# Optimization experiments

Measured on AMD Instinct MI355X. Metric: run time of the kernel, lower is better.

The kernel has to match this reference:

```python
import jax, jax.numpy as jnp
import numpy as np

B, L, LH, D, H = 32, 512, 2048, 1024, 4
DK = D // H  # dot-attn head dim
NEG = -1e9


def _ln(x, g, b, eps=1e-5):
    m = x.mean(-1, keepdims=True)
    v = ((x - m) ** 2).mean(-1, keepdims=True)
    return (x - m) / jnp.sqrt(v + eps) * g + b


def setup_inputs() -> dict:
    key = jax.random.key(0)
    ks = jax.random.split(key, 16)
    s = 0.05
    inp = {
        "seq_emb": jax.random.normal(ks[0], (B, L, D), jnp.float32),
        "seq_mask": jnp.ones((B, L), jnp.float32),
        "his_seq_emb": jax.random.normal(ks[1], (B, LH, D), jnp.float32),
        "his_seq_mask": jnp.ones((B, LH), jnp.float32),
        # dot-product MHA (bias=True)
        "sa_wq": jax.random.normal(ks[2], (D, D), jnp.float32) * s,
        "sa_bq": jnp.zeros((D,), jnp.float32),
        "sa_wk": jax.random.normal(ks[3], (D, D), jnp.float32) * s,
        "sa_bk": jnp.zeros((D,), jnp.float32),
        "sa_wv": jax.random.normal(ks[4], (D, D), jnp.float32) * s,
        "sa_bv": jnp.zeros((D,), jnp.float32),
        "sa_wo": jax.random.normal(ks[5], (D, D), jnp.float32) * s,
        "sa_bo": jnp.zeros((D,), jnp.float32),
        # short LayerNorm
        "sn_g": jnp.ones((D,), jnp.float32),
        "sn_b": jnp.zeros((D,), jnp.float32),
        # additive MHA (h=1, bias=False)
        "aa_wq": jax.random.normal(ks[6], (D, D), jnp.float32) * s,
        "aa_wk": jax.random.normal(ks[7], (D, D), jnp.float32) * s,
        "aa_wv": jax.random.normal(ks[8], (D, D), jnp.float32) * s,
        "aa_wo": jax.random.normal(ks[9], (D, D), jnp.float32) * s,
        "aa_wa": jax.random.normal(ks[10], (D,), jnp.float32) * s,
        # long LayerNorm
        "ln_g": jnp.ones((D,), jnp.float32),
        "ln_b": jnp.zeros((D,), jnp.float32),
    }
    return inp


def reference(seq_emb, seq_mask, his_seq_emb, his_seq_mask,
              sa_wq, sa_bq, sa_wk, sa_bk, sa_wv, sa_bv, sa_wo, sa_bo,
              sn_g, sn_b, aa_wq, aa_wk, aa_wv, aa_wo, aa_wa, ln_g, ln_b):
    # ---- dot-product self attention over seq_emb (dropout = eval/no-op) ----
    def split_heads(x):  # (B,L,D) -> (B,H,L,DK)
        return x.reshape(B, -1, H, DK).transpose(0, 2, 1, 3)

    q = split_heads(seq_emb @ sa_wq + sa_bq)
    k = split_heads(seq_emb @ sa_wk + sa_bk)
    v = split_heads(seq_emb @ sa_wv + sa_bv)
    scores = jnp.einsum('bhqd,bhkd->bhqk', q, k) / jnp.sqrt(jnp.float32(DK))
    scores = jnp.where(seq_mask[:, None, None, :] == 0, NEG, scores)
    p_attn = jax.nn.softmax(scores, axis=-1)  # (B,H,L,L)
    ctx = jnp.einsum('bhqk,bhkd->bhqd', p_attn, v)
    ctx = ctx.transpose(0, 2, 1, 3).reshape(B, L, D)
    sa_out = ctx @ sa_wo + sa_bo

    poi_attn = _ln(sa_out, sn_g, sn_b) * seq_mask[:, :, None]
    poi_hidden = poi_attn.mean(axis=1, keepdims=True)  # (B,1,D)

    # ---- additive (Bahdanau) attention, h=1, Lq=1 ----
    aq = poi_hidden @ aa_wq        # (B,1,D)
    ak = his_seq_emb @ aa_wk       # (B,LH,D)
    av = his_seq_emb @ aa_wv       # (B,LH,D)
    feats = jnp.tanh(aq[:, :, None, :] + ak[:, None, :, :])  # (B,1,LH,D)
    a_scores = jnp.einsum('bqkd,d->bqk', feats, aa_wa)        # (B,1,LH)
    a_scores = jnp.where(his_seq_mask[:, None, :] == 0, NEG, a_scores)
    a_w = jax.nn.softmax(a_scores, axis=-1)
    a_ctx = jnp.einsum('bqk,bkd->bqd', a_w, av)               # (B,1,D)
    aa_out = a_ctx @ aa_wo

    his_poi_hidden = poi_hidden + _ln(aa_out, ln_g, ln_b)     # (B,1,D)

    attn_weight = p_attn[:, 0, :, :]                          # (B,L,L)
    seq_hidden = jnp.concatenate([poi_hidden, his_poi_hidden], axis=-1)[:, 0, :]  # (B,2D)
    return seq_hidden, attn_weight
```

## Files before the change

kernel.cpp:

```cpp
#include <hip/hip_runtime.h>

#define NEGV (-1000000000.0f)

typedef __attribute__((ext_vector_type(8))) short sh8;
typedef __attribute__((ext_vector_type(4))) short sh4;
typedef __attribute__((ext_vector_type(8))) __bf16 bf16x8;
typedef __attribute__((ext_vector_type(4))) float f32x4;

__device__ __forceinline__ float b2f(unsigned short u) {
  unsigned v = ((unsigned)u) << 16;
  return __builtin_bit_cast(float, v);
}
__device__ __forceinline__ unsigned short f2b(float f) {
  unsigned x = __builtin_bit_cast(unsigned, f);
  unsigned r = (x + 0x7fffu + ((x >> 16) & 1u)) >> 16;
  return (unsigned short)r;
}
__device__ __forceinline__ void g2l16(const void* g, void* l) {
  __builtin_amdgcn_global_load_lds((const __attribute__((address_space(1))) unsigned int*)g,
                                   (__attribute__((address_space(3))) unsigned int*)l, 16, 0, 0);
}
__device__ __forceinline__ f32x4 mfma16(bf16x8 a, bf16x8 b, f32x4 c) {
  return __builtin_amdgcn_mfma_f32_16x16x32_bf16(a, b, c, 0, 0, 0);
}
__device__ __forceinline__ float fast_tanh(float x) {
  x = fminf(fmaxf(x, -15.f), 15.f);
  float e = __expf(2.f * x);
  return (e - 1.f) / (e + 1.f);
}

__global__ void cvt_bf16(const float* __restrict__ src, unsigned short* __restrict__ dst, int n4) {
  int i = blockIdx.x * blockDim.x + threadIdx.x;
  int stride = gridDim.x * blockDim.x;
  for (; i < n4; i += stride) {
    float4 v = ((const float4*)src)[i];
    sh4 o;
    o[0] = (short)f2b(v.x); o[1] = (short)f2b(v.y);
    o[2] = (short)f2b(v.z); o[3] = (short)f2b(v.w);
    ((sh4*)dst)[i] = o;
  }
}

__global__ void tcvt(const float* __restrict__ src, unsigned short* __restrict__ dst) {
  __shared__ float tile[64][65];
  int bx = blockIdx.x, by = blockIdx.y;
  int tx = threadIdx.x & 63, ty = threadIdx.x >> 6;
#pragma unroll
  for (int i = 0; i < 16; ++i) {
    int r = i * 4 + ty;
    tile[r][tx] = src[(size_t)(by * 64 + r) * 1024 + bx * 64 + tx];
  }
  __syncthreads();
#pragma unroll
  for (int i = 0; i < 16; ++i) {
    int r = i * 4 + ty;
    dst[(size_t)(bx * 64 + r) * 1024 + by * 64 + tx] = f2b(tile[tx][r]);
  }
}

template<int EPI>
__global__ __launch_bounds__(512, 1)
void gemm256(const unsigned short* __restrict__ A, const unsigned short* __restrict__ Bt,
             int nbx,
             const float* __restrict__ b0, const float* __restrict__ b1,
             const float* __restrict__ b2,
             unsigned short* __restrict__ O0, unsigned short* __restrict__ O1,
             unsigned short* __restrict__ O2,
             const float* __restrict__ aq, const float* __restrict__ wa,
             float* __restrict__ sc)
{
  __shared__ char lds[131072];
  const int tid = threadIdx.x;
  const int w = tid >> 6, l = tid & 63;
  const int wm = w >> 2, wn = w & 3;
  const int lr = l & 15, g = l >> 4;
  const int kg16 = g * 16;

  const int wg = blockIdx.x;
  const int cpx = gridDim.x >> 3;
  const int wgid = (wg & 7) * cpx + (wg >> 3);
  const int bx = wgid % nbx, by = wgid / nbx;
  const size_t m0 = (size_t)by * 256;
  const int n0 = bx * 256;

  f32x4 acc[8][4] = {};

  const int srow = tid >> 2, sk = (tid & 3) * 8;
  const unsigned short* gA = A + (m0 + srow) * 1024 + sk;
  const unsigned short* gB = Bt + ((size_t)n0 + srow) * 1024 + sk;
  char* const sbase = lds + w * 1024;

  const int aoff = (wm * 128 + lr) * 64 + kg16;
  const int boff = 16384 + (wn * 64 + lr) * 64 + kg16;

#pragma unroll
  for (int p = 0; p < 2; ++p) {
    const unsigned short* a = gA + p * 32;
    const unsigned short* b = gB + p * 32;
    char* base = sbase + (p << 15);
    g2l16(a, base);
    g2l16(a + 128 * 1024, base + 8192);
    g2l16(b, base + 16384);
    g2l16(b + 128 * 1024, base + 24576);
  }
  asm volatile("s_waitcnt vmcnt(4)" ::: "memory");
  __builtin_amdgcn_s_barrier();

#pragma unroll 1
  for (int kt = 0; kt < 32; ++kt) {
    const char* pb = lds + ((kt & 3) << 15);
    char* nb = sbase + (((kt + 2) & 3) << 15);
    bf16x8 af[4], bf[4];

    if (kt < 30) {
      const unsigned short* a = gA + (kt + 2) * 32;
      g2l16(a, nb);
      g2l16(a + 128 * 1024, nb + 8192);
    }
#pragma unroll
    for (int j = 0; j < 4; ++j) bf[j] = *(const bf16x8*)(pb + boff + j * 1024);
#pragma unroll
    for (int i = 0; i < 4; ++i) af[i] = *(const bf16x8*)(pb + aoff + i * 1024);
    __builtin_amdgcn_s_barrier();
    asm volatile("s_waitcnt lgkmcnt(0)" ::: "memory");
    __builtin_amdgcn_sched_barrier(0);
    __builtin_amdgcn_s_setprio(1);
#pragma unroll
    for (int i = 0; i < 4; ++i)
#pragma unroll
      for (int j = 0; j < 4; ++j)
        acc[i][j] = mfma16(af[i], bf[j], acc[i][j]);
    __builtin_amdgcn_s_setprio(0);
    __builtin_amdgcn_s_barrier();

    if (kt < 30) {
      const unsigned short* b = gB + (kt + 2) * 32;
      g2l16(b, nb + 16384);
      g2l16(b + 128 * 1024, nb + 24576);
    }
#pragma unroll
    for (int i = 0; i < 4; ++i) af[i] = *(const bf16x8*)(pb + aoff + (4 + i) * 1024);
    __builtin_amdgcn_s_barrier();
    asm volatile("s_waitcnt lgkmcnt(0)" ::: "memory");
    __builtin_amdgcn_sched_barrier(0);
    __builtin_amdgcn_s_setprio(1);
#pragma unroll
    for (int i = 0; i < 4; ++i)
#pragma unroll
      for (int j = 0; j < 4; ++j)
        acc[4 + i][j] = mfma16(af[i], bf[j], acc[4 + i][j]);
    __builtin_amdgcn_s_setprio(0);
    if (kt < 30) {
      asm volatile("s_waitcnt vmcnt(4)" ::: "memory");
    } else if (kt == 30) {
      asm volatile("s_waitcnt vmcnt(0)" ::: "memory");
    }
    __builtin_amdgcn_s_barrier();
  }

  if (EPI == 0) {
#pragma unroll
    for (int j = 0; j < 4; ++j) {
      int col = n0 + wn * 64 + j * 16 + lr;
      float bv = b0[col];
#pragma unroll
      for (int i = 0; i < 8; ++i) {
        size_t rowb = m0 + wm * 128 + i * 16 + g * 4;
#pragma unroll
        for (int r = 0; r < 4; ++r)
          O0[(rowb + r) * 1024 + col] = f2b(acc[i][j][r] + bv);
      }
    }
  } else if (EPI == 1) {
#pragma unroll
    for (int j = 0; j < 4; ++j) {
      int col3 = n0 + wn * 64 + j * 16 + lr;
      int part = col3 >> 10, c = col3 & 1023;
      float bv = (part == 0) ? b0[c] : (part == 1) ? b1[c] : b2[c];
      if (part < 2) {
        unsigned short* O = part == 0 ? O0 : O1;
#pragma unroll
        for (int i = 0; i < 8; ++i) {
          size_t rowb = m0 + wm * 128 + i * 16 + g * 4;
#pragma unroll
          for (int r = 0; r < 4; ++r)
            O[(rowb + r) * 1024 + c] = f2b(acc[i][j][r] + bv);
        }
      } else {
        int h = c >> 8, d = c & 255;
#pragma unroll
        for (int i = 0; i < 8; ++i) {
          size_t row = m0 + wm * 128 + i * 16 + g * 4;
          int bb = (int)(row >> 9), ll = (int)(row & 511);
          size_t base = ((size_t)(bb * 4 + h) * 256 + d) * 512 + ll;
#pragma unroll
          for (int r = 0; r < 4; ++r)
            O2[base + r] = f2b(acc[i][j][r] + bv);
        }
      }
    }
  } else {
    const int bb = (int)(m0 >> 11);
#pragma unroll
    for (int i = 0; i < 8; ++i) {
      float rp[4] = {0.f, 0.f, 0.f, 0.f};
#pragma unroll
      for (int j = 0; j < 4; ++j) {
        int col = n0 + wn * 64 + j * 16 + lr;
        float wav = wa[col];
        float aqv = aq[bb * 1024 + col];
#pragma unroll
        for (int r = 0; r < 4; ++r)
          rp[r] += wav * fast_tanh(acc[i][j][r] + aqv);
      }
#pragma unroll
      for (int off = 1; off < 16; off <<= 1)
#pragma unroll
        for (int r = 0; r < 4; ++r)
          rp[r] += __shfl_xor(rp[r], off, 64);
      if (lr == 0) {
        size_t rowb = m0 + wm * 128 + i * 16 + g * 4;
#pragma unroll
        for (int r = 0; r < 4; ++r)
          atomicAdd(&sc[rowb + r], rp[r]);
      }
    }
  }
}

__global__ __launch_bounds__(256, 4)
void attn_kernel(const unsigned short* __restrict__ q, const unsigned short* __restrict__ k,
                 const unsigned short* __restrict__ vT, const float* __restrict__ seq_mask,
                 unsigned short* __restrict__ ctx, float* __restrict__ attn_out)
{
  __shared__ char smem[34304];
  unsigned short* Qs = (unsigned short*)smem;
  unsigned short* Ps = (unsigned short*)smem;
  float* redm = (float*)(smem + 33280);
  float* reds = (float*)(smem + 33792);
  const int t = threadIdx.x, w = t >> 6, l = t & 63;
  const int lr = l & 15, g = l >> 4, lk8 = g * 8;
  const int wg = blockIdx.x;
  const int wgid = (wg & 7) * 256 + (wg >> 3);
  const int qt = wgid & 15, bh = wgid >> 4;
  const int h = bh & 3, b = bh >> 2;
  const int l0 = qt * 32;

  for (int idx = t; idx < 32 * 32; idx += 256) {
    int r = idx >> 5, ch = (idx & 31) * 8;
    *(sh8*)&Qs[r * 264 + ch] =
        *(const sh8*)&q[((size_t)(b * 512 + l0 + r)) * 1024 + h * 256 + ch];
  }
  __syncthreads();

  f32x4 accs[2][8] = {};
  const unsigned short* kbase = k + ((size_t)b * 512) * 1024 + h * 256;
#pragma unroll
  for (int ds = 0; ds < 8; ++ds) {
    int d0 = ds * 32;
    bf16x8 a0 = *(const bf16x8*)&Qs[lr * 264 + d0 + lk8];
    bf16x8 a1 = *(const bf16x8*)&Qs[(16 + lr) * 264 + d0 + lk8];
#pragma unroll
    for (int j = 0; j < 8; ++j) {
      int kj = w * 128 + j * 16 + lr;
      bf16x8 bb = *(const bf16x8*)&kbase[(size_t)kj * 1024 + d0 + lk8];
      accs[0][j] = mfma16(a0, bb, accs[0][j]);
      accs[1][j] = mfma16(a1, bb, accs[1][j]);
    }
  }

#pragma unroll
  for (int j = 0; j < 8; ++j) {
    int col = w * 128 + j * 16 + lr;
    float mv = seq_mask[b * 512 + col];
    bool msk = (mv == 0.f);
#pragma unroll
    for (int i = 0; i < 2; ++i)
#pragma unroll
      for (int r = 0; r < 4; ++r)
        accs[i][j][r] = msk ? NEGV : accs[i][j][r] * 0.0625f;
  }

  float mx[2][4], sm[2][4];
#pragma unroll
  for (int i = 0; i < 2; ++i)
#pragma unroll
    for (int r = 0; r < 4; ++r) {
      float m = accs[i][0][r];
#pragma unroll
      for (int j = 1; j < 8; ++j) m = fmaxf(m, accs[i][j][r]);
      mx[i][r] = m;
    }
#pragma unroll
  for (int off = 1; off < 16; off <<= 1)
#pragma unroll
    for (int i = 0; i < 2; ++i)
#pragma unroll
      for (int r = 0; r < 4; ++r)
        mx[i][r] = fmaxf(mx[i][r], __shfl_xor(mx[i][r], off, 64));
  if (lr == 0) {
#pragma unroll
    for (int i = 0; i < 2; ++i)
#pragma unroll
      for (int r = 0; r < 4; ++r)
        redm[w * 32 + i * 16 + g * 4 + r] = mx[i][r];
  }
  __syncthreads();
#pragma unroll
  for (int i = 0; i < 2; ++i)
#pragma unroll
    for (int r = 0; r < 4; ++r) {
      int row = i * 16 + g * 4 + r;
      mx[i][r] = fmaxf(fmaxf(redm[row], redm[32 + row]),
                       fmaxf(redm[64 + row], redm[96 + row]));
      sm[i][r] = 0.f;
    }

#pragma unroll
  for (int i = 0; i < 2; ++i)
#pragma unroll
    for (int j = 0; j < 8; ++j)
#pragma unroll
      for (int r = 0; r < 4; ++r) {
        float p = __expf(accs[i][j][r] - mx[i][r]);
        accs[i][j][r] = p;
        sm[i][r] += p;
      }
#pragma unroll
  for (int off = 1; off < 16; off <<= 1)
#pragma unroll
    for (int i = 0; i < 2; ++i)
#pragma unroll
      for (int r = 0; r < 4; ++r)
        sm[i][r] += __shfl_xor(sm[i][r], off, 64);
  if (lr == 0) {
#pragma unroll
    for (int i = 0; i < 2; ++i)
#pragma unroll
      for (int r = 0; r < 4; ++r)
        reds[w * 32 + i * 16 + g * 4 + r] = sm[i][r];
  }
  __syncthreads();
#pragma unroll
  for (int i = 0; i < 2; ++i)
#pragma unroll
    for (int r = 0; r < 4; ++r) {
      int row = i * 16 + g * 4 + r;
      float s = reds[row] + reds[32 + row] + reds[64 + row] + reds[96 + row];
      sm[i][r] = 1.f / s;
    }

#pragma unroll
  for (int i = 0; i < 2; ++i)
#pragma unroll
    for (int j = 0; j < 8; ++j) {
      int col = w * 128 + j * 16 + lr;
#pragma unroll
      for (int r = 0; r < 4; ++r) {
        int row = i * 16 + g * 4 + r;
        float pn = accs[i][j][r] * sm[i][r];
        Ps[row * 520 + col] = f2b(pn);
        if (h == 0)
          attn_out[((size_t)(b * 512 + l0 + row)) * 512 + col] = pn;
      }
    }
  __syncthreads();

  f32x4 acco[2][4] = {};
  const unsigned short* vbase = vT + ((size_t)(b * 4 + h)) * 256 * 512;
#pragma unroll
  for (int ks = 0; ks < 16; ++ks) {
    int kj0 = ks * 32;
    bf16x8 a0 = *(const bf16x8*)&Ps[lr * 520 + kj0 + lk8];
    bf16x8 a1 = *(const bf16x8*)&Ps[(16 + lr) * 520 + kj0 + lk8];
#pragma unroll
    for (int j = 0; j < 4; ++j) {
      int d = w * 64 + j * 16 + lr;
      bf16x8 bb = *(const bf16x8*)&vbase[(size_t)d * 512 + kj0 + lk8];
      acco[0][j] = mfma16(a0, bb, acco[0][j]);
      acco[1][j] = mfma16(a1, bb, acco[1][j]);
    }
  }
#pragma unroll
  for (int i = 0; i < 2; ++i)
#pragma unroll
    for (int j = 0; j < 4; ++j) {
      int col = w * 64 + j * 16 + lr;
#pragma unroll
      for (int r = 0; r < 4; ++r) {
        int row = i * 16 + g * 4 + r;
        ctx[((size_t)(b * 512 + l0 + row)) * 1024 + h * 256 + col] = f2b(acco[i][j][r]);
      }
    }
}

__global__ __launch_bounds__(256)
void ln_mean(const unsigned short* __restrict__ sa, const float* __restrict__ g,
             const float* __restrict__ bt, const float* __restrict__ mask,
             float* __restrict__ poi_sum)
{
  const int b = blockIdx.y, ch = blockIdx.x;
  const int t = threadIdx.x, w = t >> 6, l = t & 63;
  float gg[16], bb[16];
#pragma unroll
  for (int j = 0; j < 16; ++j) { gg[j] = g[l * 16 + j]; bb[j] = bt[l * 16 + j]; }
  float accv[16];
#pragma unroll
  for (int j = 0; j < 16; ++j) accv[j] = 0.f;
  for (int rr = 0; rr < 16; ++rr) {
    int row = ch * 64 + w * 16 + rr;
    const unsigned short* rp = sa + ((size_t)(b * 512 + row)) * 1024 + l * 16;
    float x[16];
    sh8 v0 = *(const sh8*)rp;
    sh8 v1 = *(const sh8*)(rp + 8);
#pragma unroll
    for (int j = 0; j < 8; ++j) {
      x[j] = b2f((unsigned short)v0[j]);
      x[8 + j] = b2f((unsigned short)v1[j]);
    }
    float s = 0.f, s2 = 0.f;
#pragma unroll
    for (int j = 0; j < 16; ++j) { s += x[j]; s2 += x[j] * x[j]; }
#pragma unroll
    for (int off = 1; off < 64; off <<= 1) {
      s += __shfl_xor(s, off, 64);
      s2 += __shfl_xor(s2, off, 64);
    }
    float mean = s * (1.f / 1024.f);
    float var = s2 * (1.f / 1024.f) - mean * mean;
    float rinv = rsqrtf(var + 1e-5f);
    float mk = mask[b * 512 + row];
#pragma unroll
    for (int j = 0; j < 16; ++j) accv[j] += ((x[j] - mean) * rinv * gg[j] + bb[j]) * mk;
  }
#pragma unroll
  for (int j = 0; j < 16; ++j) atomicAdd(&poi_sum[b * 1024 + l * 16 + j], accv[j]);
}

__global__ void finalize_poi(const float* __restrict__ ps, float* __restrict__ poi) {
  int i = blockIdx.x * 256 + threadIdx.x;
  if (i < 32 * 1024) poi[i] = ps[i] * (1.f / 512.f);
}

__global__ __launch_bounds__(256)
void gemv32(const float* __restrict__ in, const float* __restrict__ W, float* __restrict__ out)
{
  const int b = blockIdx.y;
  const int n = blockIdx.x * 256 + threadIdx.x;
  const float* ib = in + b * 1024;
  float acc = 0.f;
  for (int d = 0; d < 1024; d += 4) {
    acc += ib[d]     * W[(size_t)d * 1024 + n]
         + ib[d + 1] * W[(size_t)(d + 1) * 1024 + n]
         + ib[d + 2] * W[(size_t)(d + 2) * 1024 + n]
         + ib[d + 3] * W[(size_t)(d + 3) * 1024 + n];
  }
  out[b * 1024 + n] = acc;
}

__global__ __launch_bounds__(256)
void softmax_his(float* __restrict__ sc, const float* __restrict__ mask)
{
  __shared__ float red[4];
  const int b = blockIdx.x, t = threadIdx.x, w = t >> 6, l = t & 63;
  float v[8];
  float mx = -3.0e38f;
#pragma unroll
  for (int i = 0; i < 8; ++i) {
    int kk = t + i * 256;
    float s = (mask[b * 2048 + kk] == 0.f) ? NEGV : sc[b * 2048 + kk];
    v[i] = s;
    mx = fmaxf(mx, s);
  }
#pragma unroll
  for (int off = 1; off < 64; off <<= 1) mx = fmaxf(mx, __shfl_xor(mx, off, 64));
  if (l == 0) red[w] = mx;
  __syncthreads();
  mx = fmaxf(fmaxf(red[0], red[1]), fmaxf(red[2], red[3]));
  float sum = 0.f;
#pragma unroll
  for (int i = 0; i < 8; ++i) { v[i] = __expf(v[i] - mx); sum += v[i]; }
#pragma unroll
  for (int off = 1; off < 64; off <<= 1) sum += __shfl_xor(sum, off, 64);
  __syncthreads();
  if (l == 0) red[w] = sum;
  __syncthreads();
  sum = red[0] + red[1] + red[2] + red[3];
  float inv = 1.f / sum;
#pragma unroll
  for (int i = 0; i < 8; ++i) sc[b * 2048 + t + i * 256] = v[i] * inv;
}

__global__ __launch_bounds__(256)
void hw_kernel(const float* __restrict__ aw, const unsigned short* __restrict__ his,
               float* __restrict__ hw)
{
  const int b = blockIdx.y, kc = blockIdx.x, t = threadIdx.x;
  const int cb = t * 4;
  float a0 = 0.f, a1 = 0.f, a2 = 0.f, a3 = 0.f;
  for (int kk = 0; kk < 256; ++kk) {
    int k = kc * 256 + kk;
    float wg = aw[b * 2048 + k];
    sh4 vv = *(const sh4*)&his[((size_t)(b * 2048 + k)) * 1024 + cb];
    a0 += wg * b2f((unsigned short)vv[0]);
    a1 += wg * b2f((unsigned short)vv[1]);
    a2 += wg * b2f((unsigned short)vv[2]);
    a3 += wg * b2f((unsigned short)vv[3]);
  }
  atomicAdd(&hw[b * 1024 + cb + 0], a0);
  atomicAdd(&hw[b * 1024 + cb + 1], a1);
  atomicAdd(&hw[b * 1024 + cb + 2], a2);
  atomicAdd(&hw[b * 1024 + cb + 3], a3);
}

__global__ __launch_bounds__(256)
void final_kernel(const float* __restrict__ aa_out, const float* __restrict__ g,
                  const float* __restrict__ bt, const float* __restrict__ poi,
                  float* __restrict__ out)
{
  __shared__ float r1[4], r2[4];
  const int b = blockIdx.x, t = threadIdx.x, w = t >> 6, l = t & 63;
  float x[4];
#pragma unroll
  for (int j = 0; j < 4; ++j) x[j] = aa_out[b * 1024 + t * 4 + j];
  float s = 0.f, s2 = 0.f;
#pragma unroll
  for (int j = 0; j < 4; ++j) { s += x[j]; s2 += x[j] * x[j]; }
#pragma unroll
  for (int off = 1; off < 64; off <<= 1) {
    s += __shfl_xor(s, off, 64);
    s2 += __shfl_xor(s2, off, 64);
  }
  if (l == 0) { r1[w] = s; r2[w] = s2; }
  __syncthreads();
  s = r1[0] + r1[1] + r1[2] + r1[3];
  s2 = r2[0] + r2[1] + r2[2] + r2[3];
  float mean = s * (1.f / 1024.f);
  float var = s2 * (1.f / 1024.f) - mean * mean;
  float rinv = rsqrtf(var + 1e-5f);
#pragma unroll
  for (int j = 0; j < 4; ++j) {
    int c = t * 4 + j;
    float lnv = (x[j] - mean) * rinv * g[c] + bt[c];
    float pv = poi[b * 1024 + c];
    out[b * 2048 + c] = pv;
    out[b * 2048 + 1024 + c] = pv + lnv;
  }
}

extern "C" void kernel_launch(void* const* d_in, const int* in_sizes, int n_in,
                              void* d_out, int out_size, void* d_ws, size_t ws_size,
                              hipStream_t stream)
{
  const float* seq_emb  = (const float*)d_in[0];
  const float* seq_mask = (const float*)d_in[1];
  const float* his_emb  = (const float*)d_in[2];
  const float* his_mask = (const float*)d_in[3];
  const float* sa_wq = (const float*)d_in[4];
  const float* sa_bq = (const float*)d_in[5];
  const float* sa_wk = (const float*)d_in[6];
  const float* sa_bk = (const float*)d_in[7];
  const float* sa_wv = (const float*)d_in[8];
  const float* sa_bv = (const float*)d_in[9];
  const float* sa_wo = (const float*)d_in[10];
  const float* sa_bo = (const float*)d_in[11];
  const float* sn_g  = (const float*)d_in[12];
  const float* sn_b  = (const float*)d_in[13];
  const float* aa_wq = (const float*)d_in[14];
  const float* aa_wk = (const float*)d_in[15];
  const float* aa_wv = (const float*)d_in[16];
  const float* aa_wo = (const float*)d_in[17];
  const float* aa_wa = (const float*)d_in[18];
  const float* ln_g  = (const float*)d_in[19];
  const float* ln_b  = (const float*)d_in[20];
  float* out = (float*)d_out;

  char* p = (char*)d_ws;
  size_t off = 0;
  auto alloc = [&](size_t bytes) -> void* {
    void* r = p + off;
    off += (bytes + 255) & ~(size_t)255;
    return r;
  };
  unsigned short* seqb = (unsigned short*)alloc((size_t)16384 * 1024 * 2);
  unsigned short* hisb = (unsigned short*)alloc((size_t)65536 * 1024 * 2);
  unsigned short* wcat = (unsigned short*)alloc((size_t)3072 * 1024 * 2);
  unsigned short* woT  = (unsigned short*)alloc((size_t)1024 * 1024 * 2);
  unsigned short* awkT = (unsigned short*)alloc((size_t)1024 * 1024 * 2);
  unsigned short* qb   = (unsigned short*)alloc((size_t)16384 * 1024 * 2);
  unsigned short* kb   = (unsigned short*)alloc((size_t)16384 * 1024 * 2);
  unsigned short* vTb  = (unsigned short*)alloc((size_t)16384 * 1024 * 2);
  unsigned short* ctxb = (unsigned short*)alloc((size_t)16384 * 1024 * 2);
  unsigned short* saob = (unsigned short*)alloc((size_t)16384 * 1024 * 2);
  float* poi_sum = (float*)alloc((size_t)32 * 1024 * 4);
  float* poi     = (float*)alloc((size_t)32 * 1024 * 4);
  float* aqb     = (float*)alloc((size_t)32 * 1024 * 4);
  float* ascore  = (float*)alloc((size_t)32 * 2048 * 4);
  float* hwb     = (float*)alloc((size_t)32 * 1024 * 4);
  float* actx    = (float*)alloc((size_t)32 * 1024 * 4);
  float* aaout   = (float*)alloc((size_t)32 * 1024 * 4);
  if (off > ws_size) return;

  hipMemsetAsync(poi_sum, 0, (size_t)32 * 1024 * 4, stream);
  hipMemsetAsync(ascore, 0, (size_t)32 * 2048 * 4, stream);
  hipMemsetAsync(hwb, 0, (size_t)32 * 1024 * 4, stream);

  cvt_bf16<<<2048, 256, 0, stream>>>(seq_emb, seqb, 16384 * 1024 / 4);
  cvt_bf16<<<2048, 256, 0, stream>>>(his_emb, hisb, 65536 * 1024 / 4);
  dim3 tg(16, 16);
  tcvt<<<tg, 256, 0, stream>>>(sa_wq, wcat);
  tcvt<<<tg, 256, 0, stream>>>(sa_wk, wcat + (size_t)1024 * 1024);
  tcvt<<<tg, 256, 0, stream>>>(sa_wv, wcat + (size_t)2048 * 1024);
  tcvt<<<tg, 256, 0, stream>>>(sa_wo, woT);
  tcvt<<<tg, 256, 0, stream>>>(aa_wk, awkT);

  gemm256<1><<<768, 512, 0, stream>>>(seqb, wcat, 12, sa_bq, sa_bk, sa_bv,
                                      qb, kb, vTb, nullptr, nullptr, nullptr);

  attn_kernel<<<2048, 256, 0, stream>>>(qb, kb, vTb, seq_mask, ctxb, out + 65536);

  gemm256<0><<<256, 512, 0, stream>>>(ctxb, woT, 4, sa_bo, nullptr, nullptr,
                                      saob, nullptr, nullptr, nullptr, nullptr, nullptr);
  ln_mean<<<dim3(8, 32), 256, 0, stream>>>(saob, sn_g, sn_b, seq_mask, poi_sum);
  finalize_poi<<<128, 256, 0, stream>>>(poi_sum, poi);
  gemv32<<<dim3(4, 32), 256, 0, stream>>>(poi, aa_wq, aqb);

  gemm256<2><<<1024, 512, 0, stream>>>(hisb, awkT, 4, nullptr, nullptr, nullptr,
                                       nullptr, nullptr, nullptr, aqb, aa_wa, ascore);
  softmax_his<<<32, 256, 0, stream>>>(ascore, his_mask);
  hw_kernel<<<dim3(8, 32), 256, 0, stream>>>(ascore, hisb, hwb);
  gemv32<<<dim3(4, 32), 256, 0, stream>>>(hwb, aa_wv, actx);
  gemv32<<<dim3(4, 32), 256, 0, stream>>>(actx, aa_wo, aaout);
  final_kernel<<<32, 256, 0, stream>>>(aaout, ln_g, ln_b, poi, out);
}
```

Measured before the change: 822.5 us.

## Swizzle GEMM LDS layout and prefetch next k-tile fragments across barrier

```diff
diff --git a/kernel.cpp b/kernel.cpp
--- a/kernel.cpp
+++ b/kernel.cpp
@@ -74,7 +74,7 @@
   const int w = tid >> 6, l = tid & 63;
   const int wm = w >> 2, wn = w & 3;
   const int lr = l & 15, g = l >> 4;
-  const int kg16 = g * 16;
+  const int swz = (lr >> 1) & 3;
 
   const int wg = blockIdx.x;
   const int cpx = gridDim.x >> 3;
@@ -85,44 +85,51 @@
 
   f32x4 acc[8][4] = {};
 
-  const int srow = tid >> 2, sk = (tid & 3) * 8;
+  const int srow = tid >> 2;
+  const int sk = (((tid & 3) ^ ((tid >> 3) & 3)) * 8);
   const unsigned short* gA = A + (m0 + srow) * 1024 + sk;
   const unsigned short* gB = Bt + ((size_t)n0 + srow) * 1024 + sk;
   char* const sbase = lds + w * 1024;
 
-  const int aoff = (wm * 128 + lr) * 64 + kg16;
-  const int boff = 16384 + (wn * 64 + lr) * 64 + kg16;
-
-#pragma unroll
-  for (int p = 0; p < 2; ++p) {
-    const unsigned short* a = gA + p * 32;
-    const unsigned short* b = gB + p * 32;
-    char* base = sbase + (p << 15);
+  const int aoff = (wm * 128 + lr) * 64 + ((g ^ swz) * 16);
+  const int boff = 16384 + (wn * 64 + lr) * 64 + ((g ^ swz) * 16);
+
+  bf16x8 af[4], bf[4], af2[4];
+
+  auto stageA = [&](int kt) {
+    const unsigned short* a = gA + kt * 32;
+    char* base = sbase + ((kt & 3) << 15);
     g2l16(a, base);
     g2l16(a + 128 * 1024, base + 8192);
+  };
+  auto stageB = [&](int kt) {
+    const unsigned short* b = gB + kt * 32;
+    char* base = sbase + ((kt & 3) << 15);
     g2l16(b, base + 16384);
     g2l16(b + 128 * 1024, base + 24576);
-  }
+  };
+  auto loadFirst = [&](int kt) {
+    const char* pb = lds + ((kt & 3) << 15);
+#pragma unroll
+    for (int j = 0; j < 4; ++j) bf[j] = *(const bf16x8*)(pb + boff + j * 1024);
+#pragma unroll
+    for (int i = 0; i < 4; ++i) af[i] = *(const bf16x8*)(pb + aoff + i * 1024);
+  };
+
+  stageA(0); stageB(0); stageA(1); stageB(1);
   asm volatile("s_waitcnt vmcnt(4)" ::: "memory");
   __builtin_amdgcn_s_barrier();
+  __builtin_amdgcn_sched_barrier(0);
+  loadFirst(0);
+  __builtin_amdgcn_sched_barrier(0);
 
 #pragma unroll 1
   for (int kt = 0; kt < 32; ++kt) {
     const char* pb = lds + ((kt & 3) << 15);
-    char* nb = sbase + (((kt + 2) & 3) << 15);
-    bf16x8 af[4], bf[4];
-
-    if (kt < 30) {
-      const unsigned short* a = gA + (kt + 2) * 32;
-      g2l16(a, nb);
-      g2l16(a + 128 * 1024, nb + 8192);
-    }
-#pragma unroll
-    for (int j = 0; j < 4; ++j) bf[j] = *(const bf16x8*)(pb + boff + j * 1024);
-#pragma unroll
-    for (int i = 0; i < 4; ++i) af[i] = *(const bf16x8*)(pb + aoff + i * 1024);
-    __builtin_amdgcn_s_barrier();
-    asm volatile("s_waitcnt lgkmcnt(0)" ::: "memory");
+    if (kt < 30) stageA(kt + 2);
+#pragma unroll
+    for (int i = 0; i < 4; ++i) af2[i] = *(const bf16x8*)(pb + aoff + (4 + i) * 1024);
+    if (kt < 30) stageB(kt + 2);
     __builtin_amdgcn_sched_barrier(0);
     __builtin_amdgcn_s_setprio(1);
 #pragma unroll
@@ -131,24 +138,12 @@
       for (int j = 0; j < 4; ++j)
         acc[i][j] = mfma16(af[i], bf[j], acc[i][j]);
     __builtin_amdgcn_s_setprio(0);
-    __builtin_amdgcn_s_barrier();
-
-    if (kt < 30) {
-      const unsigned short* b = gB + (kt + 2) * 32;
-      g2l16(b, nb + 16384);
-      g2l16(b + 128 * 1024, nb + 24576);
-    }
-#pragma unroll
-    for (int i = 0; i < 4; ++i) af[i] = *(const bf16x8*)(pb + aoff + (4 + i) * 1024);
-    __builtin_amdgcn_s_barrier();
-    asm volatile("s_waitcnt lgkmcnt(0)" ::: "memory");
-    __builtin_amdgcn_sched_barrier(0);
     __builtin_amdgcn_s_setprio(1);
 #pragma unroll
     for (int i = 0; i < 4; ++i)
 #pragma unroll
       for (int j = 0; j < 4; ++j)
-        acc[4 + i][j] = mfma16(af[i], bf[j], acc[4 + i][j]);
+        acc[4 + i][j] = mfma16(af2[i], bf[j], acc[4 + i][j]);
     __builtin_amdgcn_s_setprio(0);
     if (kt < 30) {
       asm volatile("s_waitcnt vmcnt(4)" ::: "memory");
@@ -156,6 +151,9 @@
       asm volatile("s_waitcnt vmcnt(0)" ::: "memory");
     }
     __builtin_amdgcn_s_barrier();
+    __builtin_amdgcn_sched_barrier(0);
+    if (kt < 31) loadFirst(kt + 1);
+    __builtin_amdgcn_sched_barrier(0);
   }
 
   if (EPI == 0) {
```

Result: faster. 795.6 us (-3.3%).
